# Kernel optimization log

Hardware: AMD Instinct MI355X
Metric: run time of the kernel (lower is better)

The kernel has to match this reference:

```python
import jax, jax.numpy as jnp
import numpy as np

B, T, D = 4, 256, 1024
E, DL, TOPK, H = 16, 64, 2, 4


def setup_inputs() -> dict:
    key = jax.random.key(0)
    ks = jax.random.split(key, 12)
    n = lambda k, s: (0.02 * jax.random.normal(k, s)).astype(jnp.float32)
    return dict(
        x=jax.random.normal(ks[0], (B, T, D), dtype=jnp.float32),
        w_down=n(ks[1], (E * DL, D)),
        pos_embed=n(ks[2], (1, E, DL)),
        gp_w=n(ks[3], (DL, D)), gp_b=jnp.zeros((DL,), jnp.float32),
        attn_in_w=n(ks[4], (3 * DL, DL)), attn_in_b=jnp.zeros((3 * DL,), jnp.float32),
        attn_out_w=n(ks[5], (DL, DL)), attn_out_b=jnp.zeros((DL,), jnp.float32),
        ln_w=jnp.ones((DL,), jnp.float32), ln_b=jnp.zeros((DL,), jnp.float32),
        ls_w=n(ks[6], (1, DL)), ls_b=jnp.zeros((1,), jnp.float32),
        g1_w=n(ks[7], (2 * DL, DL)), g1_b=jnp.zeros((2 * DL,), jnp.float32),
        g2_w=n(ks[8], (E, 2 * DL)), g2_b=jnp.zeros((E,), jnp.float32),
        w_up=n(ks[9], (E, DL, D)),
    )


def reference(x, w_down, pos_embed, gp_w, gp_b, attn_in_w, attn_in_b,
              attn_out_w, attn_out_b, ln_w, ln_b, ls_w, ls_b,
              g1_w, g1_b, g2_w, g2_b, w_up):
    Bq, Tq, Dm = x.shape
    N = Bq * Tq
    xf = x.reshape(N, Dm)
    # per-token per-expert low-rank features [N, E, DL]
    ef = (xf @ w_down.T).reshape(N, E, DL)
    # global context per batch element -> [B, DL]
    gctx = x.mean(axis=1) @ gp_w.T + gp_b
    gtok = jnp.repeat(gctx, Tq, axis=0)[:, None, :]  # [N, 1, DL]
    seq = jnp.concatenate([gtok, ef + pos_embed], axis=1)  # [N, E+1, DL]
    # tiny multihead self-attention over E+1 tokens, eval mode (no dropout)
    qkv = seq @ attn_in_w.T + attn_in_b
    q, k, v = jnp.split(qkv, 3, axis=-1)
    hd = DL // H
    sh = lambda t: t.reshape(N, E + 1, H, hd).transpose(0, 2, 1, 3)
    q, k, v = sh(q), sh(k), sh(v)
    scores = jnp.einsum('nhqd,nhkd->nhqk', q, k) / np.float32(np.sqrt(hd))
    attn = jax.nn.softmax(scores, axis=-1)
    ctx = jnp.einsum('nhqk,nhkd->nhqd', attn, v).transpose(0, 2, 1, 3).reshape(N, E + 1, DL)
    attn_out = ctx @ attn_out_w.T + attn_out_b
    h = attn_out + seq
    mu = h.mean(-1, keepdims=True)
    var = h.var(-1, keepdims=True)
    hn = (h - mu) / jnp.sqrt(var + 1e-5) * ln_w + ln_b
    refined = hn[:, 1:, :]  # drop global token -> [N, E, DL]
    local_logits = (refined @ ls_w.T + ls_b)[..., 0]  # [N, E]
    gb = jax.nn.gelu(gctx @ g1_w.T + g1_b, approximate=False) @ g2_w.T + g2_b  # [B, E]
    logits = local_logits + jnp.repeat(gb, Tq, axis=0)
    probs = jax.nn.softmax(logits, axis=-1)
    tw, ti = jax.lax.top_k(probs, TOPK)
    tw = tw / tw.sum(-1, keepdims=True)
    sel = jnp.take_along_axis(ef, ti[..., None], axis=1)  # [N, K, DL]
    act = jax.nn.gelu(sel, approximate=False)
    # gather per-token expert up-projections and batched vec-mat
    eo = jnp.einsum('nkd,nkdm->nkm', act, w_up[ti])  # [N, K, D]
    out = (eo * tw[..., None]).sum(axis=1).reshape(Bq, Tq, Dm)
    mean_prob = probs.mean(axis=0)
    one_hot = jnp.zeros_like(probs).at[jnp.arange(N)[:, None], ti].set(1.0)
    aux_loss = E * jnp.sum(mean_prob * one_hot.mean(axis=0))
    return out, aux_loss
```

## Files before the change

kernel.cpp:

```cpp
#include <hip/hip_runtime.h>
#include <math.h>

#define NB 4
#define TT 256
#define DMODEL 1024
#define NE 16
#define DLQ 64
#define NH 4
#define HD 16
#define SEQL 17
#define NTOK 1024

static constexpr size_t WS_EF    = 0;
static constexpr size_t WS_AH    = 1048576;
static constexpr size_t WS_AL    = 1572864;
static constexpr size_t WS_BH    = 2097152;
static constexpr size_t WS_BL    = 2621440;
static constexpr size_t WS_P1    = 3145728;
static constexpr size_t WS_ACT   = 4194304;
static constexpr size_t WS_AIWFH = 4259840;
static constexpr size_t WS_AIWFL = 4265984;
static constexpr size_t WS_AOWFH = 4272128;
static constexpr size_t WS_AOWFL = 4274176;
static constexpr size_t WS_G1FH  = 4276224;
static constexpr size_t WS_G1FL  = 4280320;
static constexpr size_t WS_PR    = 4308992;
static constexpr size_t WS_TI    = 4325376;
static constexpr size_t WS_GCTX  = 4326400;
static constexpr size_t WS_XPART = 4465664;

typedef __attribute__((ext_vector_type(8))) short short8;
typedef __attribute__((ext_vector_type(4))) float f32x4;

__device__ __forceinline__ float gelu_exact(float x) {
    return 0.5f * x * (1.0f + erff(x * 0.70710678118654752f));
}

__device__ __forceinline__ unsigned short f2bf(float f) {
    unsigned int u = __float_as_uint(f);
    unsigned int r = (u + 0x7fffu + ((u >> 16) & 1u)) >> 16;
    return (unsigned short)r;
}
__device__ __forceinline__ float bf2f(unsigned short h) {
    return __uint_as_float(((unsigned int)h) << 16);
}

#define DPP_ADD(v, ctrl) { int _m = __builtin_amdgcn_update_dpp(0, __float_as_int(v), ctrl, 0xF, 0xF, true); \
                           v += __int_as_float(_m); }
__device__ __forceinline__ float rsum16(float v) {
    DPP_ADD(v, 0x128);
    DPP_ADD(v, 0x124);
    DPP_ADD(v, 0x122);
    DPP_ADD(v, 0x121);
    return v;
}
__device__ __forceinline__ float rsum64(float v) {
    v = rsum16(v);
    v += __shfl_xor(v, 16);
    v += __shfl_xor(v, 32);
    return v;
}

__global__ __launch_bounds__(256) void k_prep(const float* __restrict__ x,
                                              const float* __restrict__ wdn,
                                              const float* __restrict__ aiw,
                                              const float* __restrict__ aow,
                                              const float* __restrict__ g1w,
                                              float* __restrict__ ws) {
    int bi = blockIdx.x;
    int tid = threadIdx.x;
    if (bi < 512) {
        int which = bi >> 8;
        int tix = bi & 255;
        int nb = tix >> 4, kb = tix & 15;
        const float* src = which ? wdn : x;
        unsigned short* hp = (unsigned short*)(ws + (which ? WS_BH : WS_AH));
        unsigned short* lp = (unsigned short*)(ws + (which ? WS_BL : WS_AL));
        int w = tid >> 6, ln = tid & 63;
#pragma unroll
        for (int h = 0; h < 2; ++h) {
            int s = w * 2 + h;
            int st = s >> 1, ks = s & 1;
            int row = nb * 64 + st * 16 + (ln & 15);
            int col = kb * 64 + ks * 32 + ((ln >> 4) << 3);
            float4 v0 = *(const float4*)(src + (size_t)row * DMODEL + col);
            float4 v1 = *(const float4*)(src + (size_t)row * DMODEL + col + 4);
            float vv[8] = {v0.x, v0.y, v0.z, v0.w, v1.x, v1.y, v1.z, v1.w};
            unsigned short h8[8], l8[8];
#pragma unroll
            for (int j = 0; j < 8; ++j) {
                h8[j] = f2bf(vv[j]);
                l8[j] = f2bf(vv[j] - bf2f(h8[j]));
            }
            size_t off = (size_t)tix * 4096 + st * 1024 + ks * 512 + ln * 8;
            *(short8*)(hp + off) = *(short8*)h8;
            *(short8*)(lp + off) = *(short8*)l8;
        }
    } else if (bi == 512) {
        unsigned short* fh = (unsigned short*)(ws + WS_AIWFH);
        unsigned short* fl = (unsigned short*)(ws + WS_AIWFL);
        for (int idx = tid; idx < 12 * 2 * 64; idx += 256) {
            int nt = idx >> 7, kf = (idx >> 6) & 1, l = idx & 63;
            int row = nt * 16 + (l & 15);
            int k = kf * 32 + ((l >> 4) << 3);
            const float* src = aiw + (size_t)row * DLQ + k;
            unsigned short h8[8], l8[8];
#pragma unroll
            for (int j = 0; j < 8; ++j) {
                h8[j] = f2bf(src[j]);
                l8[j] = f2bf(src[j] - bf2f(h8[j]));
            }
            size_t off = (size_t)(nt * 2 + kf) * 512 + l * 8;
            *(short8*)(fh + off) = *(short8*)h8;
            *(short8*)(fl + off) = *(short8*)l8;
        }
        unsigned short* gh = (unsigned short*)(ws + WS_AOWFH);
        unsigned short* gl = (unsigned short*)(ws + WS_AOWFL);
        for (int idx = tid; idx < 4 * 2 * 64; idx += 256) {
            int nt = idx >> 7, kf = (idx >> 6) & 1, l = idx & 63;
            int row = nt * 16 + (l & 15);
            int k = kf * 32 + ((l >> 4) << 3);
            const float* src = aow + (size_t)row * DLQ + k;
            unsigned short h8[8], l8[8];
#pragma unroll
            for (int j = 0; j < 8; ++j) {
                h8[j] = f2bf(src[j]);
                l8[j] = f2bf(src[j] - bf2f(h8[j]));
            }
            size_t off = (size_t)(nt * 2 + kf) * 512 + l * 8;
            *(short8*)(gh + off) = *(short8*)h8;
            *(short8*)(gl + off) = *(short8*)l8;
        }
        unsigned short* qh = (unsigned short*)(ws + WS_G1FH);
        unsigned short* ql = (unsigned short*)(ws + WS_G1FL);
        for (int idx = tid; idx < 8 * 2 * 64; idx += 256) {
            int nt = idx >> 7, kf = (idx >> 6) & 1, l = idx & 63;
            int row = nt * 16 + (l & 15);
            int k = kf * 32 + ((l >> 4) << 3);
            const float* src = g1w + (size_t)row * DLQ + k;
            unsigned short h8[8], l8[8];
#pragma unroll
            for (int j = 0; j < 8; ++j) {
                h8[j] = f2bf(src[j]);
                l8[j] = f2bf(src[j] - bf2f(h8[j]));
            }
            size_t off = (size_t)(nt * 2 + kf) * 512 + l * 8;
            *(short8*)(qh + off) = *(short8*)h8;
            *(short8*)(ql + off) = *(short8*)l8;
        }
    } else {
        int idx = bi - 513;
        int b = idx >> 3, j = idx & 7;
        const float* xb = x + (size_t)(b * 256 + j * 32) * DMODEL + tid * 4;
        float4 acc = {0.f, 0.f, 0.f, 0.f};
#pragma unroll 8
        for (int r = 0; r < 32; ++r) {
            float4 v = *(const float4*)(xb + (size_t)r * DMODEL);
            acc.x += v.x; acc.y += v.y; acc.z += v.z; acc.w += v.w;
        }
        *(float4*)(ws + WS_XPART + (size_t)idx * DMODEL + tid * 4) = acc;
    }
}

__global__ __launch_bounds__(256) void k_ef_mfma(const float* __restrict__ gp_w,
                                                 const float* __restrict__ gp_b,
                                                 float* __restrict__ ws) {
    __shared__ __attribute__((aligned(16))) unsigned short smem[16384];
    int tid = threadIdx.x;
    int bi = blockIdx.x;

    if (bi >= 512) {
        int q = bi - 512;
        int wv = tid >> 6, l = tid & 63;
        float4 xa[4] = {{0.f,0.f,0.f,0.f},{0.f,0.f,0.f,0.f},
                        {0.f,0.f,0.f,0.f},{0.f,0.f,0.f,0.f}};
        const float* xp = ws + WS_XPART + (size_t)q * 8 * DMODEL + l * 16;
#pragma unroll
        for (int j = 0; j < 8; ++j) {
#pragma unroll
            for (int qq = 0; qq < 4; ++qq) {
                float4 v = *(const float4*)(xp + (size_t)j * DMODEL + qq * 4);
                xa[qq].x += v.x; xa[qq].y += v.y; xa[qq].z += v.z; xa[qq].w += v.w;
            }
        }
        float xm[16];
#pragma unroll
        for (int qq = 0; qq < 4; ++qq) {
            xm[qq * 4 + 0] = xa[qq].x * (1.0f / TT);
            xm[qq * 4 + 1] = xa[qq].y * (1.0f / TT);
            xm[qq * 4 + 2] = xa[qq].z * (1.0f / TT);
            xm[qq * 4 + 3] = xa[qq].w * (1.0f / TT);
        }
#pragma unroll 4
        for (int cq = 0; cq < 16; ++cq) {
            int c = wv * 16 + cq;
            const float* gw = gp_w + (size_t)c * DMODEL + l * 16;
            float s = 0.f;
#pragma unroll
            for (int qq = 0; qq < 4; ++qq) {
                float4 w4 = *(const float4*)(gw + qq * 4);
                s += xm[qq * 4 + 0] * w4.x + xm[qq * 4 + 1] * w4.y +
                     xm[qq * 4 + 2] * w4.z + xm[qq * 4 + 3] * w4.w;
            }
            s = rsum64(s);
            if (l == 0) ws[WS_GCTX + q * DLQ + c] = s + gp_b[c];
        }
        return;
    }

    int xcd = bi & 7;
    int g   = bi >> 3;
    int kz  = g >> 5;
    int rem = g & 31;
    int nb  = (xcd >> 1) * 4 + (rem >> 3);
    int mb  = (xcd & 1) * 8 + (rem & 7);

    const unsigned short* AhP = (const unsigned short*)(ws + WS_AH);
    const unsigned short* AlP = (const unsigned short*)(ws + WS_AL);
    const unsigned short* BhP = (const unsigned short*)(ws + WS_BH);
    const unsigned short* BlP = (const unsigned short*)(ws + WS_BL);
    int w = tid >> 6, l = tid & 63;
    int wn = (w >> 1) * 32, wm = (w & 1) * 32;
    int stA = wn >> 4, stB = wm >> 4;
    f32x4 acc00 = {0.f, 0.f, 0.f, 0.f}, acc01 = acc00, acc10 = acc00, acc11 = acc00;

    for (int it = 0; it < 8; ++it) {
        int kb = kz * 8 + it;
        const char* srcs[4] = {
            (const char*)(AhP + (size_t)(nb * 16 + kb) * 4096),
            (const char*)(AlP + (size_t)(nb * 16 + kb) * 4096),
            (const char*)(BhP + (size_t)(mb * 16 + kb) * 4096),
            (const char*)(BlP + (size_t)(mb * 16 + kb) * 4096)};
#pragma unroll
        for (int p = 0; p < 4; ++p) {
#pragma unroll
            for (int h = 0; h < 2; ++h) {
                __builtin_amdgcn_global_load_lds(
                    (const __attribute__((address_space(1))) void*)(srcs[p] + h * 4096 + tid * 16),
                    (__attribute__((address_space(3))) void*)((char*)smem + p * 8192 + h * 4096 + tid * 16),
                    16, 0, 0);
            }
        }
        __syncthreads();
        const unsigned short* Ah = smem;
        const unsigned short* Al = smem + 4096;
        const unsigned short* Bh = smem + 8192;
        const unsigned short* Bl = smem + 12288;
#pragma unroll
        for (int ks = 0; ks < 2; ++ks) {
            short8 ah0 = *(const short8*)(Ah + (stA + 0) * 1024 + ks * 512 + l * 8);
            short8 ah1 = *(const short8*)(Ah + (stA + 1) * 1024 + ks * 512 + l * 8);
            short8 al0 = *(const short8*)(Al + (stA + 0) * 1024 + ks * 512 + l * 8);
            short8 al1 = *(const short8*)(Al + (stA + 1) * 1024 + ks * 512 + l * 8);
            short8 bh0 = *(const short8*)(Bh + (stB + 0) * 1024 + ks * 512 + l * 8);
            short8 bh1 = *(const short8*)(Bh + (stB + 1) * 1024 + ks * 512 + l * 8);
            short8 bl0 = *(const short8*)(Bl + (stB + 0) * 1024 + ks * 512 + l * 8);
            short8 bl1 = *(const short8*)(Bl + (stB + 1) * 1024 + ks * 512 + l * 8);
            acc00 = __builtin_amdgcn_mfma_f32_16x16x32_bf16(ah0, bh0, acc00, 0, 0, 0);
            acc00 = __builtin_amdgcn_mfma_f32_16x16x32_bf16(al0, bh0, acc00, 0, 0, 0);
            acc00 = __builtin_amdgcn_mfma_f32_16x16x32_bf16(ah0, bl0, acc00, 0, 0, 0);
            acc01 = __builtin_amdgcn_mfma_f32_16x16x32_bf16(ah0, bh1, acc01, 0, 0, 0);
            acc01 = __builtin_amdgcn_mfma_f32_16x16x32_bf16(al0, bh1, acc01, 0, 0, 0);
            acc01 = __builtin_amdgcn_mfma_f32_16x16x32_bf16(ah0, bl1, acc01, 0, 0, 0);
            acc10 = __builtin_amdgcn_mfma_f32_16x16x32_bf16(ah1, bh0, acc10, 0, 0, 0);
            acc10 = __builtin_amdgcn_mfma_f32_16x16x32_bf16(al1, bh0, acc10, 0, 0, 0);
            acc10 = __builtin_amdgcn_mfma_f32_16x16x32_bf16(ah1, bl0, acc10, 0, 0, 0);
            acc11 = __builtin_amdgcn_mfma_f32_16x16x32_bf16(ah1, bh1, acc11, 0, 0, 0);
            acc11 = __builtin_amdgcn_mfma_f32_16x16x32_bf16(al1, bh1, acc11, 0, 0, 0);
            acc11 = __builtin_amdgcn_mfma_f32_16x16x32_bf16(ah1, bl1, acc11, 0, 0, 0);
        }
        __syncthreads();
    }
    int cr = (l >> 4) * 4, cc = l & 15;
    int n0 = nb * 64;
    float* P = ws + (kz == 0 ? WS_EF : WS_P1);
    int m0 = mb * 64;
#pragma unroll
    for (int r = 0; r < 4; ++r) {
        P[(size_t)(n0 + wn + cr + r) * DMODEL + (m0 + wm + cc)]           = acc00[r];
        P[(size_t)(n0 + wn + cr + r) * DMODEL + (m0 + wm + 16 + cc)]      = acc01[r];
        P[(size_t)(n0 + wn + 16 + cr + r) * DMODEL + (m0 + wm + cc)]      = acc10[r];
        P[(size_t)(n0 + wn + 16 + cr + r) * DMODEL + (m0 + wm + 16 + cc)] = acc11[r];
    }
}

__global__ __launch_bounds__(256) void k_attn2(const float* __restrict__ pos_embed,
                                               const float* __restrict__ attn_in_b,
                                               const float* __restrict__ attn_out_b,
                                               const float* __restrict__ ln_w,
                                               const float* __restrict__ ln_b,
                                               const float* __restrict__ ls_w,
                                               const float* __restrict__ ls_b,
                                               const float* __restrict__ g1_b,
                                               const float* __restrict__ g2_w,
                                               const float* __restrict__ g2_b,
                                               float* __restrict__ ws) {
    int n = blockIdx.x;
    int w = threadIdx.x >> 6;
    int l = threadIdx.x & 63;
    int b = n >> 8;

    __shared__ float qkv[SEQL * 200];
    __shared__ __attribute__((aligned(16))) char ubuf[8192];
    __shared__ __attribute__((aligned(16))) unsigned short ctxH[1024];
    __shared__ __attribute__((aligned(16))) unsigned short ctxL[1024];
    __shared__ float lgv_sh[NE];
    __shared__ float hsh[128];
    unsigned short* sH = (unsigned short*)ubuf;
    unsigned short* sL = (unsigned short*)(ubuf + 4096);
    float* ao = (float*)ubuf;

    float seqc[SEQL];
    float gcv = ws[WS_GCTX + b * DLQ + l];
    {
        const float* efp0 = ws + WS_EF + (size_t)n * DMODEL;
        const float* efp1 = ws + WS_P1 + (size_t)n * DMODEL;
#pragma unroll
        for (int i = 0; i < SEQL; ++i) {
            float s = (i == 0) ? gcv
                               : efp0[(i - 1) * DLQ + l] + efp1[(i - 1) * DLQ + l] +
                                 pos_embed[(i - 1) * DLQ + l];
            seqc[i] = s;
            int lo_r = w * 5, hi_r = w * 5 + 4;
            if (i >= lo_r && i <= hi_r) {
                unsigned short hs = f2bf(s);
                unsigned short lsv = f2bf(s - bf2f(hs));
                int mt = i >> 4;
                int ls = (i & 15) + (((l >> 3) & 3) << 4);
                int kf = l >> 5;
                int j = l & 7;
                size_t off = (size_t)(mt * 2 + kf) * 512 + ls * 8 + j;
                sH[off] = hs;
                sL[off] = lsv;
            }
        }
    }
    __syncthreads();

    {
        const unsigned short* fh = (const unsigned short*)(ws + WS_AIWFH);
        const unsigned short* fl = (const unsigned short*)(ws + WS_AIWFL);
        const unsigned short* qh = (const unsigned short*)(ws + WS_G1FH);
        const unsigned short* ql = (const unsigned short*)(ws + WS_G1FL);
        f32x4 acc[3][2];
        f32x4 accg[2];
#pragma unroll
        for (int t = 0; t < 3; ++t)
#pragma unroll
            for (int m = 0; m < 2; ++m) acc[t][m] = (f32x4){0.f, 0.f, 0.f, 0.f};
#pragma unroll
        for (int t = 0; t < 2; ++t) accg[t] = (f32x4){0.f, 0.f, 0.f, 0.f};
#pragma unroll
        for (int kf = 0; kf < 2; ++kf) {
            short8 ah0 = *(const short8*)(sH + (0 * 2 + kf) * 512 + l * 8);
            short8 ah1 = *(const short8*)(sH + (1 * 2 + kf) * 512 + l * 8);
            short8 al0 = *(const short8*)(sL + (0 * 2 + kf) * 512 + l * 8);
            short8 al1 = *(const short8*)(sL + (1 * 2 + kf) * 512 + l * 8);
#pragma unroll
            for (int t = 0; t < 3; ++t) {
                int nt = w * 3 + t;
                short8 bh = *(const short8*)(fh + (size_t)(nt * 2 + kf) * 512 + l * 8);
                short8 bl = *(const short8*)(fl + (size_t)(nt * 2 + kf) * 512 + l * 8);
                acc[t][0] = __builtin_amdgcn_mfma_f32_16x16x32_bf16(ah0, bh, acc[t][0], 0, 0, 0);
                acc[t][0] = __builtin_amdgcn_mfma_f32_16x16x32_bf16(al0, bh, acc[t][0], 0, 0, 0);
                acc[t][0] = __builtin_amdgcn_mfma_f32_16x16x32_bf16(ah0, bl, acc[t][0], 0, 0, 0);
                acc[t][1] = __builtin_amdgcn_mfma_f32_16x16x32_bf16(ah1, bh, acc[t][1], 0, 0, 0);
                acc[t][1] = __builtin_amdgcn_mfma_f32_16x16x32_bf16(al1, bh, acc[t][1], 0, 0, 0);
                acc[t][1] = __builtin_amdgcn_mfma_f32_16x16x32_bf16(ah1, bl, acc[t][1], 0, 0, 0);
            }
#pragma unroll
            for (int t = 0; t < 2; ++t) {
                int nt = w * 2 + t;
                short8 bh = *(const short8*)(qh + (size_t)(nt * 2 + kf) * 512 + l * 8);
                short8 bl = *(const short8*)(ql + (size_t)(nt * 2 + kf) * 512 + l * 8);
                accg[t] = __builtin_amdgcn_mfma_f32_16x16x32_bf16(ah0, bh, accg[t], 0, 0, 0);
                accg[t] = __builtin_amdgcn_mfma_f32_16x16x32_bf16(al0, bh, accg[t], 0, 0, 0);
                accg[t] = __builtin_amdgcn_mfma_f32_16x16x32_bf16(ah0, bl, accg[t], 0, 0, 0);
            }
        }
#pragma unroll
        for (int t = 0; t < 3; ++t) {
            int col = (w * 3 + t) * 16 + (l & 15);
            float bias = attn_in_b[col];
#pragma unroll
            for (int r = 0; r < 4; ++r) {
                int row = (l >> 4) * 4 + r;
                qkv[row * 200 + col] = acc[t][0][r] + bias;
            }
            if ((l >> 4) == 0) qkv[16 * 200 + col] = acc[t][1][0] + bias;
        }
#pragma unroll
        for (int t = 0; t < 2; ++t) {
            int col = (w * 2 + t) * 16 + (l & 15);
            if ((l >> 4) == 0) hsh[col] = accg[t][0] + g1_b[col];
        }
    }
    __syncthreads();

    {
        int g = l >> 4;
        float kc[SEQL], vc[SEQL];
#pragma unroll
        for (int j = 0; j < SEQL; ++j) {
            kc[j] = qkv[j * 200 + 64 + g * 16 + (l & 15)];
            vc[j] = qkv[j * 200 + 128 + l];
        }
        for (int i = w * 4 + 1; i <= w * 4 + 4; ++i) {
            float qi = qkv[i * 200 + g * 16 + (l & 15)];
            float sj[SEQL];
#pragma unroll
            for (int j = 0; j < SEQL; ++j) {
                sj[j] = rsum16(qi * kc[j]) * 0.25f;
            }
            float m = sj[0];
#pragma unroll
            for (int j = 1; j < SEQL; ++j) m = fmaxf(m, sj[j]);
            float ssum = 0.f;
#pragma unroll
            for (int j = 0; j < SEQL; ++j) { sj[j] = __expf(sj[j] - m); ssum += sj[j]; }
            float inv = 1.f / ssum;
            float c = 0.f;
#pragma unroll
            for (int j = 0; j < SEQL; ++j) c += sj[j] * vc[j];
            c *= inv;
            unsigned short ch = f2bf(c);
            unsigned short cl = f2bf(c - bf2f(ch));
            int ls = ((i - 1) & 15) + (((l >> 3) & 3) << 4);
            int kf = l >> 5;
            int j2 = l & 7;
            size_t off = (size_t)kf * 512 + ls * 8 + j2;
            ctxH[off] = ch;
            ctxL[off] = cl;
        }
    }
    __syncthreads();

    {
        const unsigned short* gh = (const unsigned short*)(ws + WS_AOWFH);
        const unsigned short* gl = (const unsigned short*)(ws + WS_AOWFL);
        f32x4 acc0 = {0.f, 0.f, 0.f, 0.f};
#pragma unroll
        for (int kf = 0; kf < 2; ++kf) {
            short8 ah = *(const short8*)(ctxH + kf * 512 + l * 8);
            short8 al = *(const short8*)(ctxL + kf * 512 + l * 8);
            short8 bh = *(const short8*)(gh + (size_t)(w * 2 + kf) * 512 + l * 8);
            short8 bl = *(const short8*)(gl + (size_t)(w * 2 + kf) * 512 + l * 8);
            acc0 = __builtin_amdgcn_mfma_f32_16x16x32_bf16(ah, bh, acc0, 0, 0, 0);
            acc0 = __builtin_amdgcn_mfma_f32_16x16x32_bf16(al, bh, acc0, 0, 0, 0);
            acc0 = __builtin_amdgcn_mfma_f32_16x16x32_bf16(ah, bl, acc0, 0, 0, 0);
        }
        __syncthreads();
        {
            int col = w * 16 + (l & 15);
            float bias = attn_out_b[col];
#pragma unroll
            for (int r = 0; r < 4; ++r) {
                int row = (l >> 4) * 4 + r;
                ao[row * 72 + col] = acc0[r] + bias;
            }
        }
    }
    __syncthreads();

    float gbv[4];
    {
        float h0 = gelu_exact(hsh[2 * l]);
        float h1 = gelu_exact(hsh[2 * l + 1]);
#pragma unroll
        for (int oo = 0; oo < 4; ++oo) {
            int o = w * 4 + oo;
            gbv[oo] = rsum64(h0 * g2_w[(size_t)o * 128 + 2 * l] +
                             h1 * g2_w[(size_t)o * 128 + 2 * l + 1]) + g2_b[o];
        }
    }

    float rs[SEQL];
#pragma unroll
    for (int i = 1; i < SEQL; ++i) rs[i] = seqc[i] + ao[(i - 1) * 72 + l];

    float c1 = ln_w[l] * ls_w[l];
    float c1sum = rsum64(c1);
    float c0sum = rsum64(ln_b[l] * ls_w[l]);
    float lsb0 = ls_b[0];
#pragma unroll
    for (int ee = 0; ee < 4; ++ee) {
        int e = w * 4 + ee;
        float x = rs[e + 1];
        float s1 = rsum64(x);
        float s2 = rsum64(x * x);
        float s3 = rsum64(x * c1);
        float mu = s1 * (1.0f / DLQ);
        float var = s2 * (1.0f / DLQ) - mu * mu;
        float rstd = rsqrtf(var + 1e-5f);
        float lgv = rstd * (s3 - mu * c1sum) + c0sum + lsb0 + gbv[ee];
        if (l == 0) lgv_sh[e] = lgv;
    }
    __syncthreads();

    if (w == 0) {
        float p[NE];
        float lgv[NE];
#pragma unroll
        for (int e = 0; e < NE; ++e) lgv[e] = lgv_sh[e];
        float m = lgv[0];
#pragma unroll
        for (int e = 1; e < NE; ++e) m = fmaxf(m, lgv[e]);
        float ssum = 0.f;
#pragma unroll
        for (int e = 0; e < NE; ++e) { p[e] = __expf(lgv[e] - m); ssum += p[e]; }
        float inv = 1.f / ssum;
#pragma unroll
        for (int e = 0; e < NE; ++e) p[e] *= inv;
        int t0 = 0; float b0 = p[0];
#pragma unroll
        for (int e = 1; e < NE; ++e) if (p[e] > b0) { b0 = p[e]; t0 = e; }
        int t1 = -1; float b1 = -1.f;
#pragma unroll
        for (int e = 0; e < NE; ++e) if (e != t0 && p[e] > b1) { b1 = p[e]; t1 = e; }

        float sw = b0 + b1;
        float tw0 = b0 / sw, tw1 = b1 / sw;
        unsigned short* actp = (unsigned short*)(ws + WS_ACT);
        float efv0 = ws[WS_EF + (size_t)n * DMODEL + t0 * DLQ + l] +
                     ws[WS_P1 + (size_t)n * DMODEL + t0 * DLQ + l];
        float efv1 = ws[WS_EF + (size_t)n * DMODEL + t1 * DLQ + l] +
                     ws[WS_P1 + (size_t)n * DMODEL + t1 * DLQ + l];
        actp[(size_t)(n * 2 + 0) * 64 + l] = f2bf(gelu_exact(efv0) * tw0);
        actp[(size_t)(n * 2 + 1) * 64 + l] = f2bf(gelu_exact(efv1) * tw1);
        if (l == 0) {
#pragma unroll
            for (int e = 0; e < NE; ++e) ws[WS_PR + (size_t)n * NE + e] = p[e];
            ((int*)(ws + WS_TI))[n] = t0 | (t1 << 8);
        }
    }
}

__global__ __launch_bounds__(256) void k_moe_gemm(const float* __restrict__ w_up,
                                                  float* __restrict__ ws,
                                                  float* __restrict__ out) {
    __shared__ int lst[2048];
    __shared__ int lcnt;
    __shared__ float wsum[4][NE];
    __shared__ int hist[NE];
    int tid = threadIdx.x;
    int wv = tid >> 6, l = tid & 63;

    if (blockIdx.x == NE) {
        if (blockIdx.y != 0) return;
        if (tid < NE) hist[tid] = 0;
        __syncthreads();
        {
            const int* tip = (const int*)(ws + WS_TI);
#pragma unroll
            for (int c = 0; c < 4; ++c) {
                int pk = tip[tid * 4 + c];
                atomicAdd(&hist[pk & 0xff], 1);
                atomicAdd(&hist[(pk >> 8) & 0xff], 1);
            }
        }
        float p[NE];
#pragma unroll
        for (int e = 0; e < NE; ++e) p[e] = 0.f;
        const float* pr = ws + WS_PR + (size_t)tid * 64;
#pragma unroll
        for (int r = 0; r < 4; ++r)
#pragma unroll
            for (int q = 0; q < 4; ++q) {
                float4 v = *(const float4*)(pr + r * 16 + q * 4);
                p[q * 4 + 0] += v.x; p[q * 4 + 1] += v.y;
                p[q * 4 + 2] += v.z; p[q * 4 + 3] += v.w;
            }
#pragma unroll
        for (int e = 0; e < NE; ++e) p[e] = rsum64(p[e]);
        if (l == 0) {
#pragma unroll
            for (int e = 0; e < NE; ++e) wsum[wv][e] = p[e];
        }
        __syncthreads();
        if (tid == 0) {
            float s = 0.f;
#pragma unroll
            for (int e = 0; e < NE; ++e) {
                float sp = wsum[0][e] + wsum[1][e] + wsum[2][e] + wsum[3][e];
                s += sp * (float)hist[e];
            }
            out[(size_t)NTOK * DMODEL] = (float)NE * s / ((float)NTOK * (float)NTOK);
        }
        return;
    }

    int e = blockIdx.x, ct = blockIdx.y;
    if (tid == 0) lcnt = 0;
    __syncthreads();
    {
        const int* tip = (const int*)(ws + WS_TI);
#pragma unroll
        for (int c = 0; c < 4; ++c) {
            int tok = wv * 256 + c * 64 + l;
            int pk = tip[tok];
            bool m1 = ((pk >> 8) & 0xff) == e;
            bool m = ((pk & 0xff) == e) || m1;
            unsigned long long mask = __ballot(m);
            int base = 0;
            if (l == 0 && mask) base = atomicAdd(&lcnt, __popcll(mask));
            base = __shfl(base, 0);
            if (m) {
                int pos = base + __popcll(mask & ((1ull << l) - 1ull));
                lst[pos] = tok * 2 + (m1 ? 1 : 0);
            }
        }
    }
    __syncthreads();
    int cnt = lcnt;
    if (cnt == 0) return;

    int col = ct * 64 + wv * 16 + (l & 15);
    int kb = (l >> 4) * 8;
    const float* wue = w_up + (size_t)e * DLQ * DMODEL + col;
    unsigned short b0v[8], b1v[8];
#pragma unroll
    for (int j = 0; j < 8; ++j) {
        b0v[j] = f2bf(wue[(size_t)(kb + j) * DMODEL]);
        b1v[j] = f2bf(wue[(size_t)(kb + 32 + j) * DMODEL]);
    }
    short8 bf0 = *(short8*)b0v;
    short8 bf1 = *(short8*)b1v;

    const unsigned short* actp = (const unsigned short*)(ws + WS_ACT);
    int cr = (l >> 4) * 4;

    for (int mt = 0; mt < cnt; mt += 16) {
        int row = mt + (l & 15);
        short8 a0 = {0, 0, 0, 0, 0, 0, 0, 0};
        short8 a1 = {0, 0, 0, 0, 0, 0, 0, 0};
        if (row < cnt) {
            int pk = lst[row];
            a0 = *(const short8*)(actp + (size_t)pk * 64 + kb);
            a1 = *(const short8*)(actp + (size_t)pk * 64 + 32 + kb);
        }
        f32x4 acc = {0.f, 0.f, 0.f, 0.f};
        acc = __builtin_amdgcn_mfma_f32_16x16x32_bf16(a0, bf0, acc, 0, 0, 0);
        acc = __builtin_amdgcn_mfma_f32_16x16x32_bf16(a1, bf1, acc, 0, 0, 0);
#pragma unroll
        for (int r = 0; r < 4; ++r) {
            int rr = mt + cr + r;
            if (rr < cnt) {
                int pk = lst[rr];
                atomicAdd(&out[(size_t)(pk >> 1) * DMODEL + col], acc[r]);
            }
        }
    }
}

extern "C" void kernel_launch(void* const* d_in, const int* in_sizes, int n_in,
                              void* d_out, int out_size, void* d_ws, size_t ws_size,
                              hipStream_t stream) {
    const float* x          = (const float*)d_in[0];
    const float* w_down     = (const float*)d_in[1];
    const float* pos_embed  = (const float*)d_in[2];
    const float* gp_w       = (const float*)d_in[3];
    const float* gp_b       = (const float*)d_in[4];
    const float* attn_in_w  = (const float*)d_in[5];
    const float* attn_in_b  = (const float*)d_in[6];
    const float* attn_out_w = (const float*)d_in[7];
    const float* attn_out_b = (const float*)d_in[8];
    const float* ln_w       = (const float*)d_in[9];
    const float* ln_b       = (const float*)d_in[10];
    const float* ls_w       = (const float*)d_in[11];
    const float* ls_b       = (const float*)d_in[12];
    const float* g1_w       = (const float*)d_in[13];
    const float* g1_b       = (const float*)d_in[14];
    const float* g2_w       = (const float*)d_in[15];
    const float* g2_b       = (const float*)d_in[16];
    const float* w_up       = (const float*)d_in[17];
    float* ws  = (float*)d_ws;
    float* out = (float*)d_out;

    hipMemsetAsync(out, 0, (size_t)out_size * sizeof(float), stream);
    k_prep<<<545, 256, 0, stream>>>(x, w_down, attn_in_w, attn_out_w, g1_w, ws);
    k_ef_mfma<<<516, 256, 0, stream>>>(gp_w, gp_b, ws);
    k_attn2<<<NTOK, 256, 0, stream>>>(pos_embed, attn_in_b, attn_out_b,
                                      ln_w, ln_b, ls_w, ls_b,
                                      g1_b, g2_w, g2_b, ws);
    k_moe_gemm<<<dim3(NE + 1, 16), 256, 0, stream>>>(w_up, ws, out);
}
```

Measured before the change: 163.9 us.

## Fuse bf16 split conversion and mean pooling into the MFMA GEMM kernel

Removes the separate prep kernel. The GEMM blocks now load fp32 x and w_down tiles directly, split each value into bf16 hi/lo parts in registers and write them to LDS. This drops the round trip through global memory for the hi/lo workspace and one kernel launch. The global-context mean is now computed by four blocks that each reduce all 256 rows, replacing the partial-sum stage. In exchange, the async global-to-LDS loads become synchronous register loads, the conversion is repeated across blocks that share a tile, and the four mean blocks may become a long tail.

```diff
diff --git a/kernel.cpp b/kernel.cpp
--- a/kernel.cpp
+++ b/kernel.cpp
@@ -12,10 +12,6 @@
 #define NTOK 1024
 
 static constexpr size_t WS_EF    = 0;
-static constexpr size_t WS_AH    = 1048576;
-static constexpr size_t WS_AL    = 1572864;
-static constexpr size_t WS_BH    = 2097152;
-static constexpr size_t WS_BL    = 2621440;
 static constexpr size_t WS_P1    = 3145728;
 static constexpr size_t WS_ACT   = 4194304;
 static constexpr size_t WS_AIWFH = 4259840;
@@ -27,7 +23,6 @@
 static constexpr size_t WS_PR    = 4308992;
 static constexpr size_t WS_TI    = 4325376;
 static constexpr size_t WS_GCTX  = 4326400;
-static constexpr size_t WS_XPART = 4465664;
 
 typedef __attribute__((ext_vector_type(8))) short short8;
 typedef __attribute__((ext_vector_type(4))) float f32x4;
@@ -61,42 +56,65 @@
     return v;
 }
 
-__global__ __launch_bounds__(256) void k_prep(const float* __restrict__ x,
-                                              const float* __restrict__ wdn,
-                                              const float* __restrict__ aiw,
-                                              const float* __restrict__ aow,
-                                              const float* __restrict__ g1w,
-                                              float* __restrict__ ws) {
+__global__ __launch_bounds__(256) void k_ef_mfma(const float* __restrict__ x,
+                                                 const float* __restrict__ wdn,
+                                                 const float* __restrict__ aiw,
+                                                 const float* __restrict__ aow,
+                                                 const float* __restrict__ g1w,
+                                                 const float* __restrict__ gp_w,
+                                                 const float* __restrict__ gp_b,
+                                                 float* __restrict__ ws) {
+    __shared__ __attribute__((aligned(16))) unsigned short smem[16384];
+    int tid = threadIdx.x;
     int bi = blockIdx.x;
-    int tid = threadIdx.x;
-    if (bi < 512) {
-        int which = bi >> 8;
-        int tix = bi & 255;
-        int nb = tix >> 4, kb = tix & 15;
-        const float* src = which ? wdn : x;
-        unsigned short* hp = (unsigned short*)(ws + (which ? WS_BH : WS_AH));
-        unsigned short* lp = (unsigned short*)(ws + (which ? WS_BL : WS_AL));
-        int w = tid >> 6, ln = tid & 63;
-#pragma unroll
-        for (int h = 0; h < 2; ++h) {
-            int s = w * 2 + h;
-            int st = s >> 1, ks = s & 1;
-            int row = nb * 64 + st * 16 + (ln & 15);
-            int col = kb * 64 + ks * 32 + ((ln >> 4) << 3);
-            float4 v0 = *(const float4*)(src + (size_t)row * DMODEL + col);
-            float4 v1 = *(const float4*)(src + (size_t)row * DMODEL + col + 4);
-            float vv[8] = {v0.x, v0.y, v0.z, v0.w, v1.x, v1.y, v1.z, v1.w};
-            unsigned short h8[8], l8[8];
-#pragma unroll
-            for (int j = 0; j < 8; ++j) {
-                h8[j] = f2bf(vv[j]);
-                l8[j] = f2bf(vv[j] - bf2f(h8[j]));
-            }
-            size_t off = (size_t)tix * 4096 + st * 1024 + ks * 512 + ln * 8;
-            *(short8*)(hp + off) = *(short8*)h8;
-            *(short8*)(lp + off) = *(short8*)l8;
-        }
-    } else if (bi == 512) {
+
+    if (bi >= 512 && bi < 516) {
+        int q = bi - 512;
+        int wv = tid >> 6, l = tid & 63;
+        float* shf = (float*)smem;
+        float4 xa[4] = {{0.f,0.f,0.f,0.f},{0.f,0.f,0.f,0.f},
+                        {0.f,0.f,0.f,0.f},{0.f,0.f,0.f,0.f}};
+        const float* xb = x + (size_t)(q * 256 + wv * 64) * DMODEL + l * 16;
+#pragma unroll 4
+        for (int r = 0; r < 64; ++r) {
+#pragma unroll
+            for (int qq = 0; qq < 4; ++qq) {
+                float4 v = *(const float4*)(xb + (size_t)r * DMODEL + qq * 4);
+                xa[qq].x += v.x; xa[qq].y += v.y; xa[qq].z += v.z; xa[qq].w += v.w;
+            }
+        }
+#pragma unroll
+        for (int qq = 0; qq < 4; ++qq)
+            *(float4*)(shf + wv * 1024 + l * 16 + qq * 4) = xa[qq];
+        __syncthreads();
+        float xm[16];
+#pragma unroll
+        for (int qq = 0; qq < 4; ++qq) {
+#pragma unroll
+            for (int k = 0; k < 4; ++k) {
+                int c = l * 16 + qq * 4 + k;
+                xm[qq * 4 + k] = (shf[c] + shf[1024 + c] + shf[2048 + c] +
+                                  shf[3072 + c]) * (1.0f / TT);
+            }
+        }
+#pragma unroll 4
+        for (int cq = 0; cq < 16; ++cq) {
+            int c = wv * 16 + cq;
+            const float* gw = gp_w + (size_t)c * DMODEL + l * 16;
+            float s = 0.f;
+#pragma unroll
+            for (int qq = 0; qq < 4; ++qq) {
+                float4 w4 = *(const float4*)(gw + qq * 4);
+                s += xm[qq * 4 + 0] * w4.x + xm[qq * 4 + 1] * w4.y +
+                     xm[qq * 4 + 2] * w4.z + xm[qq * 4 + 3] * w4.w;
+            }
+            s = rsum64(s);
+            if (l == 0) ws[WS_GCTX + q * DLQ + c] = s + gp_b[c];
+        }
+        return;
+    }
+
+    if (bi == 516) {
         unsigned short* fh = (unsigned short*)(ws + WS_AIWFH);
         unsigned short* fl = (unsigned short*)(ws + WS_AIWFL);
         for (int idx = tid; idx < 12 * 2 * 64; idx += 256) {
@@ -148,63 +166,6 @@
             *(short8*)(qh + off) = *(short8*)h8;
             *(short8*)(ql + off) = *(short8*)l8;
         }
-    } else {
-        int idx = bi - 513;
-        int b = idx >> 3, j = idx & 7;
-        const float* xb = x + (size_t)(b * 256 + j * 32) * DMODEL + tid * 4;
-        float4 acc = {0.f, 0.f, 0.f, 0.f};
-#pragma unroll 8
-        for (int r = 0; r < 32; ++r) {
-            float4 v = *(const float4*)(xb + (size_t)r * DMODEL);
-            acc.x += v.x; acc.y += v.y; acc.z += v.z; acc.w += v.w;
-        }
-        *(float4*)(ws + WS_XPART + (size_t)idx * DMODEL + tid * 4) = acc;
-    }
-}
-
-__global__ __launch_bounds__(256) void k_ef_mfma(const float* __restrict__ gp_w,
-                                                 const float* __restrict__ gp_b,
-                                                 float* __restrict__ ws) {
-    __shared__ __attribute__((aligned(16))) unsigned short smem[16384];
-    int tid = threadIdx.x;
-    int bi = blockIdx.x;
-
-    if (bi >= 512) {
-        int q = bi - 512;
-        int wv = tid >> 6, l = tid & 63;
-        float4 xa[4] = {{0.f,0.f,0.f,0.f},{0.f,0.f,0.f,0.f},
-                        {0.f,0.f,0.f,0.f},{0.f,0.f,0.f,0.f}};
-        const float* xp = ws + WS_XPART + (size_t)q * 8 * DMODEL + l * 16;
-#pragma unroll
-        for (int j = 0; j < 8; ++j) {
-#pragma unroll
-            for (int qq = 0; qq < 4; ++qq) {
-                float4 v = *(const float4*)(xp + (size_t)j * DMODEL + qq * 4);
-                xa[qq].x += v.x; xa[qq].y += v.y; xa[qq].z += v.z; xa[qq].w += v.w;
-            }
-        }
-        float xm[16];
-#pragma unroll
-        for (int qq = 0; qq < 4; ++qq) {
-            xm[qq * 4 + 0] = xa[qq].x * (1.0f / TT);
-            xm[qq * 4 + 1] = xa[qq].y * (1.0f / TT);
-            xm[qq * 4 + 2] = xa[qq].z * (1.0f / TT);
-            xm[qq * 4 + 3] = xa[qq].w * (1.0f / TT);
-        }
-#pragma unroll 4
-        for (int cq = 0; cq < 16; ++cq) {
-            int c = wv * 16 + cq;
-            const float* gw = gp_w + (size_t)c * DMODEL + l * 16;
-            float s = 0.f;
-#pragma unroll
-            for (int qq = 0; qq < 4; ++qq) {
-                float4 w4 = *(const float4*)(gw + qq * 4);
-                s += xm[qq * 4 + 0] * w4.x + xm[qq * 4 + 1] * w4.y +
-                     xm[qq * 4 + 2] * w4.z + xm[qq * 4 + 3] * w4.w;
-            }
-            s = rsum64(s);
-            if (l == 0) ws[WS_GCTX + q * DLQ + c] = s + gp_b[c];
-        }
         return;
     }
 
@@ -215,10 +176,6 @@
     int nb  = (xcd >> 1) * 4 + (rem >> 3);
     int mb  = (xcd & 1) * 8 + (rem & 7);
 
-    const unsigned short* AhP = (const unsigned short*)(ws + WS_AH);
-    const unsigned short* AlP = (const unsigned short*)(ws + WS_AL);
-    const unsigned short* BhP = (const unsigned short*)(ws + WS_BH);
-    const unsigned short* BlP = (const unsigned short*)(ws + WS_BL);
     int w = tid >> 6, l = tid & 63;
     int wn = (w >> 1) * 32, wm = (w & 1) * 32;
     int stA = wn >> 4, stB = wm >> 4;
@@ -226,20 +183,31 @@
 
     for (int it = 0; it < 8; ++it) {
         int kb = kz * 8 + it;
-        const char* srcs[4] = {
-            (const char*)(AhP + (size_t)(nb * 16 + kb) * 4096),
-            (const char*)(AlP + (size_t)(nb * 16 + kb) * 4096),
-            (const char*)(BhP + (size_t)(mb * 16 + kb) * 4096),
-            (const char*)(BlP + (size_t)(mb * 16 + kb) * 4096)};
-#pragma unroll
-        for (int p = 0; p < 4; ++p) {
-#pragma unroll
-            for (int h = 0; h < 2; ++h) {
-                __builtin_amdgcn_global_load_lds(
-                    (const __attribute__((address_space(1))) void*)(srcs[p] + h * 4096 + tid * 16),
-                    (__attribute__((address_space(3))) void*)((char*)smem + p * 8192 + h * 4096 + tid * 16),
-                    16, 0, 0);
-            }
+#pragma unroll
+        for (int h = 0; h < 2; ++h) {
+            int c = h * 256 + tid;
+            int r  = ((c >> 7) * 16) + (c & 15);
+            int co = (((c >> 6) & 1) * 32) + (((c >> 4) & 3) << 3);
+            const float* pa = x   + (size_t)(nb * 64 + r) * DMODEL + kb * 64 + co;
+            const float* pb = wdn + (size_t)(mb * 64 + r) * DMODEL + kb * 64 + co;
+            float4 a0 = *(const float4*)(pa);
+            float4 a1 = *(const float4*)(pa + 4);
+            float4 b0 = *(const float4*)(pb);
+            float4 b1 = *(const float4*)(pb + 4);
+            float av[8] = {a0.x, a0.y, a0.z, a0.w, a1.x, a1.y, a1.z, a1.w};
+            float bv[8] = {b0.x, b0.y, b0.z, b0.w, b1.x, b1.y, b1.z, b1.w};
+            unsigned short ah8[8], al8[8], bh8[8], bl8[8];
+#pragma unroll
+            for (int j = 0; j < 8; ++j) {
+                ah8[j] = f2bf(av[j]);
+                al8[j] = f2bf(av[j] - bf2f(ah8[j]));
+                bh8[j] = f2bf(bv[j]);
+                bl8[j] = f2bf(bv[j] - bf2f(bh8[j]));
+            }
+            *(short8*)(smem + c * 8)          = *(short8*)ah8;
+            *(short8*)(smem + 4096 + c * 8)   = *(short8*)al8;
+            *(short8*)(smem + 8192 + c * 8)   = *(short8*)bh8;
+            *(short8*)(smem + 12288 + c * 8)  = *(short8*)bl8;
         }
         __syncthreads();
         const unsigned short* Ah = smem;
@@ -677,8 +645,8 @@
     float* out = (float*)d_out;
 
     hipMemsetAsync(out, 0, (size_t)out_size * sizeof(float), stream);
-    k_prep<<<545, 256, 0, stream>>>(x, w_down, attn_in_w, attn_out_w, g1_w, ws);
-    k_ef_mfma<<<516, 256, 0, stream>>>(gp_w, gp_b, ws);
+    k_ef_mfma<<<517, 256, 0, stream>>>(x, w_down, attn_in_w, attn_out_w, g1_w,
+                                       gp_w, gp_b, ws);
     k_attn2<<<NTOK, 256, 0, stream>>>(pos_embed, attn_in_b, attn_out_b,
                                       ln_w, ln_b, ls_w, ls_b,
                                       g1_b, g2_w, g2_b, ws);
```

After: 175.4 us. 7.0% more time.
